# Performance work log

Measured on AMD Instinct MI355X. Metric: run time of the kernel, lower is better.

Reference implementation:

```python
import jax, jax.numpy as jnp
import numpy as np

ICM_ITER = 3


def setup_inputs() -> dict:
    key = jax.random.key(0)
    k1, k2, k3, k4, k5 = jax.random.split(key, 5)
    n, d, M, K = 32768, 128, 8, 256
    X = jax.random.normal(k1, (n, d), dtype=jnp.float32)
    C = jax.random.normal(k2, (M * K, d), dtype=jnp.float32)
    C_unary = jax.random.normal(k3, (n, M * K), dtype=jnp.float32)
    C_pair = jax.random.normal(k4, (M, M, K, K), dtype=jnp.float32)
    B = jax.random.randint(k5, (n, M), 0, K, dtype=jnp.int32)
    return {"X": X, "C": C, "C_unary": C_unary, "C_pair": C_pair, "B": B}


def reference(X, C, C_unary, C_pair, B):
    # Shapes: X [n,d], C [M*K,d], C_unary [n,M*K], C_pair [M,M,K,K], B [n,M]
    n = X.shape[0]
    M, _, K, _ = C_pair.shape
    # x_ci = -2 * X @ C.T, viewed as [n, M, K]
    x_ci = (-2.0 * (X @ C.T)).reshape(n, M, K)
    Cu = C_unary.reshape(n, M, K)
    j_idx = jnp.arange(M)
    # Coordinate-descent ICM: sequential over (iter, codebook m); vectorized over n.
    for _ in range(ICM_ITER):
        for i in range(M):
            # C_pair[i, j, :, B[:, j]] summed over j -> [n, K]
            # advanced indexing: dims 0 and 2 advanced, dim 1 sliced -> (n, M, K)
            pair = jnp.sum(C_pair[i][j_idx[None, :], :, B], axis=1)  # [n, K]
            scores = x_ci[:, i] + Cu[:, i] + pair                     # [n, K]
            B = B.at[:, i].set(jnp.argmin(scores, axis=1).astype(B.dtype))
    return B
```

## Files before the change

### kernel.cpp

```cpp
#include <hip/hip_runtime.h>

#define N_PTS 32768
#define DIM   128
#define M_CB  8
#define K_CB  256
#define MK    2048
#define N_ITER 3

__global__ __launch_bounds__(1024) void kpair_transpose(const float* __restrict__ Cp,
                                                        float* __restrict__ Cpt) {
    __shared__ float t[32][33];
    int ij = blockIdx.z;
    int b0 = blockIdx.x * 32, k0 = blockIdx.y * 32;
    int tx = threadIdx.x, ty = threadIdx.y;
    const size_t base = (size_t)ij * K_CB * K_CB;
    t[ty][tx] = Cp[base + (size_t)(k0 + ty) * K_CB + (b0 + tx)];
    __syncthreads();
    Cpt[base + (size_t)(b0 + ty) * K_CB + (k0 + tx)] = t[tx][ty];
}

__global__ __launch_bounds__(256) void kgemm(const float* __restrict__ X,
                                             const float* __restrict__ C,
                                             const float* __restrict__ Cu,
                                             float* __restrict__ S, int n0) {
    __shared__ float As[8][128];
    __shared__ float Bs[8][128];
    const int t  = threadIdx.x;
    const int tx = t & 15;
    const int ty = t >> 4;
    const int c0 = blockIdx.x * 128;
    const int p0 = blockIdx.y * 128;

    float acc[8][8];
#pragma unroll
    for (int i = 0; i < 8; ++i)
#pragma unroll
        for (int j = 0; j < 8; ++j) acc[i][j] = 0.f;

    const int lp = t & 127;
    const int lg = t >> 7;
    const float* xsrc = X + (size_t)(n0 + p0 + lp) * DIM + lg * 4;
    const float* csrc = C + (size_t)(c0 + lp) * DIM + lg * 4;

    for (int s = 0; s < 16; ++s) {
        float4 xa = *(const float4*)(xsrc + s * 8);
        float4 cb = *(const float4*)(csrc + s * 8);
        __syncthreads();
        As[lg * 4 + 0][lp] = xa.x; As[lg * 4 + 1][lp] = xa.y;
        As[lg * 4 + 2][lp] = xa.z; As[lg * 4 + 3][lp] = xa.w;
        Bs[lg * 4 + 0][lp] = cb.x; Bs[lg * 4 + 1][lp] = cb.y;
        Bs[lg * 4 + 2][lp] = cb.z; Bs[lg * 4 + 3][lp] = cb.w;
        __syncthreads();
#pragma unroll
        for (int dd = 0; dd < 8; ++dd) {
            float4 a0 = *(const float4*)&As[dd][ty * 8];
            float4 a1 = *(const float4*)&As[dd][ty * 8 + 4];
            float4 b0 = *(const float4*)&Bs[dd][tx * 8];
            float4 b1 = *(const float4*)&Bs[dd][tx * 8 + 4];
            float a[8] = {a0.x, a0.y, a0.z, a0.w, a1.x, a1.y, a1.z, a1.w};
            float b[8] = {b0.x, b0.y, b0.z, b0.w, b1.x, b1.y, b1.z, b1.w};
#pragma unroll
            for (int pi = 0; pi < 8; ++pi)
#pragma unroll
                for (int ci = 0; ci < 8; ++ci) acc[pi][ci] += a[pi] * b[ci];
        }
    }

#pragma unroll
    for (int pi = 0; pi < 8; ++pi) {
        size_t row = (size_t)(p0 + ty * 8 + pi);
        const float* cus = Cu + ((size_t)n0 + row) * MK + c0 + tx * 8;
        float4 u0 = *(const float4*)cus;
        float4 u1 = *(const float4*)(cus + 4);
        float* dst = S + row * MK + c0 + tx * 8;
        float4 o0 = make_float4(-2.f * acc[pi][0] + u0.x, -2.f * acc[pi][1] + u0.y,
                                -2.f * acc[pi][2] + u0.z, -2.f * acc[pi][3] + u0.w);
        float4 o1 = make_float4(-2.f * acc[pi][4] + u1.x, -2.f * acc[pi][5] + u1.y,
                                -2.f * acc[pi][6] + u1.z, -2.f * acc[pi][7] + u1.w);
        *(float4*)dst = o0;
        *(float4*)(dst + 4) = o1;
    }
}

__global__ __launch_bounds__(256) void kicm(const float* __restrict__ S,
                                            const float* __restrict__ Cpt,
                                            const int* __restrict__ Bin,
                                            int* __restrict__ out, int n0) {
    const int l = threadIdx.x & 63;
    const int w = (int)((blockIdx.x * 256 + threadIdx.x) >> 6);
    const size_t n = (size_t)n0 + w;

    float4 s[8];
#pragma unroll
    for (int i = 0; i < 8; ++i)
        s[i] = *(const float4*)(S + (size_t)w * MK + i * K_CB + l * 4);

    int b[8];
#pragma unroll
    for (int j = 0; j < 8; ++j) b[j] = Bin[n * M_CB + j];

    for (int it = 0; it < N_ITER; ++it) {
#pragma unroll
        for (int i = 0; i < 8; ++i) {
            float4 r[8];
#pragma unroll
            for (int j = 0; j < 8; ++j) {
                size_t off = ((size_t)((i * M_CB + j) * K_CB + b[j])) * K_CB + l * 4;
                r[j] = *(const float4*)(Cpt + off);
            }
            float4 acc = s[i];
#pragma unroll
            for (int j = 0; j < 8; ++j) {
                acc.x += r[j].x; acc.y += r[j].y; acc.z += r[j].z; acc.w += r[j].w;
            }
            float v = acc.x; int idx = l * 4;
            if (acc.y < v) { v = acc.y; idx = l * 4 + 1; }
            if (acc.z < v) { v = acc.z; idx = l * 4 + 2; }
            if (acc.w < v) { v = acc.w; idx = l * 4 + 3; }
#pragma unroll
            for (int off = 32; off > 0; off >>= 1) {
                float ov = __shfl_down(v, off);
                int   oi = __shfl_down(idx, off);
                if (ov < v || (ov == v && oi < idx)) { v = ov; idx = oi; }
            }
            idx = __shfl(idx, 0);
            b[i] = idx;
        }
    }

    if (l == 0) {
        int4 o0 = make_int4(b[0], b[1], b[2], b[3]);
        int4 o1 = make_int4(b[4], b[5], b[6], b[7]);
        *(int4*)(out + n * M_CB)     = o0;
        *(int4*)(out + n * M_CB + 4) = o1;
    }
}

extern "C" void kernel_launch(void* const* d_in, const int* in_sizes, int n_in,
                              void* d_out, int out_size, void* d_ws, size_t ws_size,
                              hipStream_t stream) {
    const float* X  = (const float*)d_in[0];
    const float* C  = (const float*)d_in[1];
    const float* Cu = (const float*)d_in[2];
    const float* Cp = (const float*)d_in[3];
    const int*   B  = (const int*)d_in[4];
    int* out = (int*)d_out;

    float* wsf = (float*)d_ws;
    const size_t CPT_ELEMS = (size_t)M_CB * M_CB * K_CB * K_CB;
    float* Cpt = wsf;
    float* S   = wsf + CPT_ELEMS;

    size_t spare_bytes = ws_size > CPT_ELEMS * 4 ? ws_size - CPT_ELEMS * 4 : 0;
    long long chunk = (long long)(spare_bytes / ((size_t)MK * 4));
    if (chunk > N_PTS) chunk = N_PTS;
    chunk = (chunk / 128) * 128;
    if (chunk < 128) chunk = 128;

    kpair_transpose<<<dim3(8, 8, 64), dim3(32, 32), 0, stream>>>(Cp, Cpt);

    for (int n0 = 0; n0 < N_PTS; n0 += (int)chunk) {
        int P = (int)((N_PTS - n0 < chunk) ? (N_PTS - n0) : chunk);
        kgemm<<<dim3(MK / 128, P / 128), 256, 0, stream>>>(X, C, Cu, S, n0);
        kicm<<<P / 4, 256, 0, stream>>>(S, Cpt, B, out, n0);
    }
}
```

Measured before the change: 1.193 ms.

## Split fused ICM kernel into one launch per codebook update step

Replaces the single ICM kernel, which looped over all iterations and codebooks inside one wavefront, with a per-(iteration, codebook) kernel launched 24 times per chunk. Assignments live in the output buffer, seeded by a device-to-device copy, and each launch reads and writes them in global memory. The intent is likely lower register pressure and higher occupancy, or shorter dependency chains per launch. The cost is many more launches, plus re-reading S rows and B from global memory on every step.

```diff
diff --git a/kernel.cpp b/kernel.cpp
--- a/kernel.cpp
+++ b/kernel.cpp
@@ -82,58 +82,41 @@
     }
 }
 
-__global__ __launch_bounds__(256) void kicm(const float* __restrict__ S,
-                                            const float* __restrict__ Cpt,
-                                            const int* __restrict__ Bin,
-                                            int* __restrict__ out, int n0) {
+__global__ __launch_bounds__(256) void kupdate(const float* __restrict__ S,
+                                               const float* __restrict__ Cpt,
+                                               int* __restrict__ B,
+                                               int n0, int i) {
     const int l = threadIdx.x & 63;
     const int w = (int)((blockIdx.x * 256 + threadIdx.x) >> 6);
     const size_t n = (size_t)n0 + w;
 
-    float4 s[8];
+    const int4 b0 = *(const int4*)(B + n * M_CB);
+    const int4 b1 = *(const int4*)(B + n * M_CB + 4);
+    const int b[8] = {b0.x, b0.y, b0.z, b0.w, b1.x, b1.y, b1.z, b1.w};
+
+    float4 acc = *(const float4*)(S + (size_t)w * MK + i * K_CB + l * 4);
+    const float* cslice = Cpt + (size_t)i * M_CB * K_CB * K_CB;
+
+    float4 r[8];
 #pragma unroll
-    for (int i = 0; i < 8; ++i)
-        s[i] = *(const float4*)(S + (size_t)w * MK + i * K_CB + l * 4);
-
-    int b[8];
+    for (int j = 0; j < 8; ++j)
+        r[j] = *(const float4*)(cslice + ((size_t)(j * K_CB + b[j])) * K_CB + l * 4);
 #pragma unroll
-    for (int j = 0; j < 8; ++j) b[j] = Bin[n * M_CB + j];
-
-    for (int it = 0; it < N_ITER; ++it) {
-#pragma unroll
-        for (int i = 0; i < 8; ++i) {
-            float4 r[8];
-#pragma unroll
-            for (int j = 0; j < 8; ++j) {
-                size_t off = ((size_t)((i * M_CB + j) * K_CB + b[j])) * K_CB + l * 4;
-                r[j] = *(const float4*)(Cpt + off);
-            }
-            float4 acc = s[i];
-#pragma unroll
-            for (int j = 0; j < 8; ++j) {
-                acc.x += r[j].x; acc.y += r[j].y; acc.z += r[j].z; acc.w += r[j].w;
-            }
-            float v = acc.x; int idx = l * 4;
-            if (acc.y < v) { v = acc.y; idx = l * 4 + 1; }
-            if (acc.z < v) { v = acc.z; idx = l * 4 + 2; }
-            if (acc.w < v) { v = acc.w; idx = l * 4 + 3; }
-#pragma unroll
-            for (int off = 32; off > 0; off >>= 1) {
-                float ov = __shfl_down(v, off);
-                int   oi = __shfl_down(idx, off);
-                if (ov < v || (ov == v && oi < idx)) { v = ov; idx = oi; }
-            }
-            idx = __shfl(idx, 0);
-            b[i] = idx;
-        }
+    for (int j = 0; j < 8; ++j) {
+        acc.x += r[j].x; acc.y += r[j].y; acc.z += r[j].z; acc.w += r[j].w;
     }
 
-    if (l == 0) {
-        int4 o0 = make_int4(b[0], b[1], b[2], b[3]);
-        int4 o1 = make_int4(b[4], b[5], b[6], b[7]);
-        *(int4*)(out + n * M_CB)     = o0;
-        *(int4*)(out + n * M_CB + 4) = o1;
+    float v = acc.x; int idx = l * 4;
+    if (acc.y < v) { v = acc.y; idx = l * 4 + 1; }
+    if (acc.z < v) { v = acc.z; idx = l * 4 + 2; }
+    if (acc.w < v) { v = acc.w; idx = l * 4 + 3; }
+#pragma unroll
+    for (int off = 32; off > 0; off >>= 1) {
+        float ov = __shfl_down(v, off);
+        int   oi = __shfl_down(idx, off);
+        if (ov < v || (ov == v && oi < idx)) { v = ov; idx = oi; }
     }
+    if (l == 0) B[n * M_CB + i] = idx;
 }
 
 extern "C" void kernel_launch(void* const* d_in, const int* in_sizes, int n_in,
@@ -159,9 +142,14 @@
 
     kpair_transpose<<<dim3(8, 8, 64), dim3(32, 32), 0, stream>>>(Cp, Cpt);
 
+    hipMemcpyAsync(out, B, (size_t)N_PTS * M_CB * sizeof(int),
+                   hipMemcpyDeviceToDevice, stream);
+
     for (int n0 = 0; n0 < N_PTS; n0 += (int)chunk) {
         int P = (int)((N_PTS - n0 < chunk) ? (N_PTS - n0) : chunk);
         kgemm<<<dim3(MK / 128, P / 128), 256, 0, stream>>>(X, C, Cu, S, n0);
-        kicm<<<P / 4, 256, 0, stream>>>(S, Cpt, B, out, n0);
+        for (int it = 0; it < N_ITER; ++it)
+            for (int i = 0; i < M_CB; ++i)
+                kupdate<<<P / 4, 256, 0, stream>>>(S, Cpt, out, n0, i);
     }
 }
```

After: 995.0 us. 1.2x faster.
